# Kernel tuning notes

Hardware: AMD Instinct MI355X
Metric: run time of the kernel (lower is better)

The kernel has to match this reference:

```python
import jax, jax.numpy as jnp
import numpy as np

B, T, H, C = 1024, 1024, 128, 6  # batch, time, hidden_dim, output_dim


def setup_inputs() -> dict:
    key = jax.random.key(0)
    ks = jax.random.split(key, 16)
    xv = jax.random.normal(ks[0], (B, T, C), dtype=jnp.float32)
    m = (jax.random.uniform(ks[1], (B, T, C)) < 0.6).astype(jnp.float32)  # binary observed mask
    dt = jax.random.uniform(ks[2], (B, T, 1), dtype=jnp.float32) * 2.0    # positive time gaps
    x = jnp.concatenate([xv, m, dt], axis=-1)  # [B,T,13]
    s = 0.05
    return {
        "x": x,
        "x_mean": jnp.zeros((C,), jnp.float32),
        "decay_x_w": jnp.ones((C,), jnp.float32),
        "decay_x_b": jnp.zeros((C,), jnp.float32),
        "decay_h_w": jnp.ones((H,), jnp.float32),
        "decay_h_b": jnp.zeros((H,), jnp.float32),
        "w_ih": jax.random.normal(ks[3], (3 * H, 2 * C), jnp.float32) * s,
        "w_hh": jax.random.normal(ks[4], (3 * H, H), jnp.float32) * s,
        "b_ih": jnp.zeros((3 * H,), jnp.float32),
        "b_hh": jnp.zeros((3 * H,), jnp.float32),
        "w1": jax.random.normal(ks[5], (H, H), jnp.float32) * s,
        "b1": jnp.zeros((H,), jnp.float32),
        "w2": jax.random.normal(ks[6], (C, H), jnp.float32) * s,
        "b2": jnp.zeros((C,), jnp.float32),
        "wu1": jax.random.normal(ks[7], (H // 2, H), jnp.float32) * s,
        "bu1": jnp.zeros((H // 2,), jnp.float32),
        "wu2": jax.random.normal(ks[8], (C, H // 2), jnp.float32) * s,
        "bu2": jnp.zeros((C,), jnp.float32),
    }


def _grud_forward(x, x_mean, decay_x_w, decay_x_b, decay_h_w, decay_h_b,
                  w_ih, w_hh, b_ih, b_hh, w1, b1, w2, b2, wu1, bu1, wu2, bu2):
    xv = jnp.transpose(x[:, :, :C], (1, 0, 2))        # [T,B,C]
    m = jnp.transpose(x[:, :, C:2 * C], (1, 0, 2))    # [T,B,C]
    dt = jnp.transpose(x[:, :, 2 * C:2 * C + 1], (1, 0, 2))  # [T,B,1]

    def step(carry, inp):
        running, x_last, h = carry
        xv_t, m_t, dt_t = inp
        obs = m_t > 0.5
        running = jnp.where(obs, 0.0, running + dt_t)          # delta_t
        gamma_x = jnp.exp(-jax.nn.relu(running * decay_x_w + decay_x_b))  # [B,C]
        gamma_h = jnp.exp(-jax.nn.relu(dt_t * decay_h_w + decay_h_b))     # [B,H]
        h = gamma_h * h
        x_last = jnp.where(obs, xv_t, x_last)
        x_hat = m_t * xv_t + (1.0 - m_t) * (gamma_x * x_last + (1.0 - gamma_x) * x_mean)
        gru_in = jnp.concatenate([x_hat, m_t], axis=-1)        # [B,2C]
        gi = gru_in @ w_ih.T + b_ih                            # [B,3H]
        gh = h @ w_hh.T + b_hh                                 # [B,3H]
        i_r, i_z, i_n = jnp.split(gi, 3, axis=-1)
        h_r, h_z, h_n = jnp.split(gh, 3, axis=-1)
        r = jax.nn.sigmoid(i_r + h_r)
        z = jax.nn.sigmoid(i_z + h_z)
        n = jnp.tanh(i_n + r * h_n)
        h = (1.0 - z) * n + z * h
        pred = jax.nn.relu(h @ w1.T + b1) @ w2.T + b2
        unc = jax.nn.softplus(jax.nn.relu(h @ wu1.T + bu1) @ wu2.T + bu2)
        return (running, x_last, h), (pred, unc)

    bsz = x.shape[0]
    init = (jnp.zeros((bsz, C), x.dtype), jnp.zeros((bsz, C), x.dtype), jnp.zeros((bsz, H), x.dtype))
    _, (pred, unc) = jax.lax.scan(step, init, (xv, m, dt))
    return jnp.transpose(pred, (1, 0, 2)), jnp.transpose(unc, (1, 0, 2))


def reference(x, x_mean, decay_x_w, decay_x_b, decay_h_w, decay_h_b,
              w_ih, w_hh, b_ih, b_hh, w1, b1, w2, b2, wu1, bu1, wu2, bu2):
    return _grud_forward(x, x_mean, decay_x_w, decay_x_b, decay_h_w, decay_h_b,
                         w_ih, w_hh, b_ih, b_hh, w1, b1, w2, b2, wu1, bu1, wu2, bu2)
```

## Files before the change

### kernel.cpp

```cpp
#include <hip/hip_runtime.h>

namespace {
constexpr int NB = 1024, NT = 1024, NH = 128;
constexpr float L2E = 1.4426950408889634f;

typedef __bf16 bf16x8 __attribute__((ext_vector_type(8)));
typedef float  f32x4  __attribute__((ext_vector_type(4)));
typedef int    i32x4  __attribute__((ext_vector_type(4)));
union FRAG { i32x4 i; bf16x8 b; };

__device__ __forceinline__ unsigned short bfb(float f) {
  union { __bf16 h; unsigned short u; } c; c.h = (__bf16)f; return c.u;
}
__device__ __forceinline__ unsigned pkbf(float a, float b) {
  return (unsigned)bfb(a) | ((unsigned)bfb(b) << 16);
}
__device__ __forceinline__ unsigned long long pk4(const f32x4 v) {
  return (unsigned long long)pkbf(v[0], v[1]) |
         ((unsigned long long)pkbf(v[2], v[3]) << 32);
}
__device__ __forceinline__ float ex2(float x) { return __builtin_amdgcn_exp2f(x); }
__device__ __forceinline__ float rcp_(float x) { return __builtin_amdgcn_rcpf(x); }

__device__ __forceinline__ FRAG pk8(const float* pp, float sc) {
  FRAG f;
  #pragma unroll
  for (int j = 0; j < 4; ++j)
    f.i[j] = (int)pkbf(pp[2 * j] * sc, pp[2 * j + 1] * sc);
  return f;
}
}

#define MFMA(a, b, c) __builtin_amdgcn_mfma_f32_16x16x32_bf16(a, b, c, 0, 0, 0)
#define BAR() do { \
  asm volatile("s_waitcnt lgkmcnt(0)" ::: "memory"); \
  __builtin_amdgcn_s_barrier(); \
} while (0)

__global__ __launch_bounds__(512, 2)
void grud_combo(const float* __restrict__ x, const float* __restrict__ x_mean,
                const float* __restrict__ dxw, const float* __restrict__ dxb,
                const float* __restrict__ dhw, const float* __restrict__ dhb,
                const float* __restrict__ w_ih, const float* __restrict__ w_hh,
                const float* __restrict__ b_ih, const float* __restrict__ b_hh,
                const float* __restrict__ w1, const float* __restrict__ b1,
                const float* __restrict__ w2, const float* __restrict__ b2,
                const float* __restrict__ wu1, const float* __restrict__ bu1,
                const float* __restrict__ wu2, const float* __restrict__ bu2,
                float* __restrict__ out,
                char* __restrict__ hcur, const char* __restrict__ hprev,
                float* __restrict__ hstate, float* __restrict__ runst,
                float* __restrict__ xlst, int t0, int t0p, int Tc, int niter)
{
  __shared__ __align__(16) char lds[40960];

  const int tid = threadIdx.x;

  if (blockIdx.x < 64) {
    if (t0 >= NT) return;

    float (*xw)[16][17] = (float(*)[16][17])lds;
    unsigned short (*gin)[16][40] = (unsigned short(*)[16][40])(lds + 2176);
    char* hdL = lds + 4736;

    const int lane = tid & 63, wv = tid >> 6;
    const int lr = lane & 15, lg = lane >> 4;
    const int b0 = blockIdx.x * 16;
    const int uidx = wv * 16 + lr;
    const int uu0  = wv * 16 + 4 * lg;

    FRAG bhh[3][4], bgi[3];
    #pragma unroll
    for (int g = 0; g < 3; ++g) {
      const float sc = (g < 2) ? -L2E : 2.f * L2E;
      const int grow = g * 128 + uidx;
      const float* wrow = w_hh + (size_t)grow * NH;
      #pragma unroll
      for (int s = 0; s < 4; ++s) bhh[g][s] = pk8(wrow + 32 * s + 8 * lg, sc);
      FRAG f; f.i = i32x4{0, 0, 0, 0};
      if (lg < 2) {
        unsigned e[8];
        #pragma unroll
        for (int j = 0; j < 8; ++j) {
          const int c = 8 * lg + j; float v = 0.f;
          if (c < 12) {
            const int ch = c >> 1;
            v = ((c & 1) ? w_ih[(size_t)grow * 12 + 6 + ch]
                         : w_ih[(size_t)grow * 12 + ch]) * sc;
          } else if (c == 12) {
            v = ((g < 2) ? (b_ih[grow] + b_hh[grow]) : b_ih[grow]) * sc;
          }
          e[j] = bfb(v);
        }
        f.i[0] = (int)(e[0] | (e[1] << 16)); f.i[1] = (int)(e[2] | (e[3] << 16));
        f.i[2] = (int)(e[4] | (e[5] << 16)); f.i[3] = (int)(e[6] | (e[7] << 16));
      }
      bgi[g] = f;
    }
    f32x4 dhwV, dhbV, bhnV;
    #pragma unroll
    for (int r = 0; r < 4; ++r) {
      dhwV[r] = -L2E * dhw[uu0 + r];
      dhbV[r] = -L2E * dhb[uu0 + r];
      bhnV[r] = b_hh[256 + uu0 + r] * (2.f * L2E);
    }

    const int  item = wv * 24 + lane;
    const bool xl = (wv < 4) && (lane < 24);
    const int  xrow = item / 6, xch = item - 6 * (item / 6);
    float dxwS = 0.f, dxbS = 0.f, xm_l = 0.f, run = 0.f, xlast = 0.f;
    if (xl) {
      dxwS = -L2E * dxw[xch]; dxbS = -L2E * dxb[xch]; xm_l = x_mean[xch];
      if (t0 > 0) { run = runst[(b0 + xrow) * 6 + xch]; xlast = xlst[(b0 + xrow) * 6 + xch]; }
    }

    const bool sl = (tid >= 256) && (tid < 464);
    const int sid = tid - 256;
    const int rrow = sid / 13, rcc = sid - 13 * (sid / 13);
    const float* xbase = x + (size_t)(b0 + rrow) * (NT * 13) + rcc;

    f32x4 hn = {0.f, 0.f, 0.f, 0.f};
    if (t0 > 0) hn = *(const f32x4*)&hstate[(size_t)(b0 + lr) * NH + uu0];

    const int wOff = lr * 256 + (((2 * wv + (lg >> 1)) ^ (lr & 7)) << 4) + (lg & 1) * 8;
    int rOff[4];
    #pragma unroll
    for (int s = 0; s < 4; ++s) rOff[s] = lr * 256 + (((4 * s + lg) ^ (lr & 7)) << 4);

    for (int i = tid; i < 2 * 16 * 28; i += 512) {
      const int buf = i / 448, rem = i - 448 * buf;
      const int row = rem / 28, c = 12 + rem - 28 * (rem / 28);
      gin[buf][row][c] = (c == 12) ? (unsigned short)0x3F80 : (unsigned short)0;
    }

    const int cb0 = t0 & 1;
    if (sl) {
      xw[cb0][rrow][rcc]     = xbase[(size_t)t0 * 13];
      const int t1 = (t0 + 1 < NT) ? t0 + 1 : NT - 1;
      xw[cb0 ^ 1][rrow][rcc] = xbase[(size_t)t1 * 13];
    }
    __syncthreads();

    f32x4 hd;
    {
      const float dt0 = xw[cb0][lr][12];
      #pragma unroll
      for (int r = 0; r < 4; ++r)
        hd[r] = ex2(fminf(dt0 * dhwV[r] + dhbV[r], 0.f)) * hn[r];
      *(unsigned long long*)(hdL + cb0 * 4096 + wOff) = pk4(hd);
    }
    if (xl) {
      const float xv = xw[cb0][xrow][xch], mt = xw[cb0][xrow][6 + xch];
      const float dtv = xw[cb0][xrow][12];
      const bool obs = mt > 0.5f;
      run = obs ? 0.f : run + dtv;
      const float gx = ex2(fminf(run * dxwS + dxbS, 0.f));
      xlast = obs ? xv : xlast;
      const float xh = mt * xv + (1.f - mt) * (gx * xlast + (1.f - gx) * xm_l);
      ((unsigned*)&gin[cb0][xrow][0])[xch] = pkbf(xh, mt);
    }
    float xr2 = 0.f;
    if (sl) { const int t2 = (t0 + 2 < NT) ? t0 + 2 : NT - 1; xr2 = xbase[(size_t)t2 * 13]; }
    BAR();

    char* hwp = hcur + (((size_t)blockIdx.x * Tc) << 12) + wv * 32 + lg * 8 + lr * 256;
    const f32x4 z4 = {0.f, 0.f, 0.f, 0.f};
    const int tend = t0 + Tc;

    #pragma unroll 1
    for (int t = t0; t < tend; ++t) {
      const int p = t & 1, q = p ^ 1;

      FRAG ag; ag.i = *(const i32x4*)&gin[p][lr][8 * lg];
      FRAG ah[4];
      #pragma unroll
      for (int s = 0; s < 4; ++s)
        ah[s].i = *(const i32x4*)(hdL + p * 4096 + rOff[s]);
      const float dtn = xw[q][lr][12];

      if (sl) {
        xw[p][rrow][rcc] = xr2;
        xr2 = xbase[(size_t)((t + 3 < NT) ? t + 3 : NT - 1) * 13];
      }

      f32x4 accr = MFMA(bgi[0].b, ag.b, z4);
      f32x4 accz = MFMA(bgi[1].b, ag.b, z4);
      f32x4 ani  = MFMA(bgi[2].b, ag.b, z4);
      f32x4 anh  = z4;
      #pragma unroll
      for (int s = 0; s < 4; ++s) {
        accr = MFMA(bhh[0][s].b, ah[s].b, accr);
        accz = MFMA(bhh[1][s].b, ah[s].b, accz);
        anh  = MFMA(bhh[2][s].b, ah[s].b, anh);
      }

      f32x4 hbv = anh + bhnV;
      #pragma unroll
      for (int r = 0; r < 4; ++r) {
        const float Er = ex2(accr[r]);
        const float rr = rcp_(1.f + Er);
        const float na = __builtin_fmaf(rr, hbv[r], ani[r]);
        const float En = ex2(na);
        const float Ez = ex2(accz[r]);
        const float em1 = En - 1.f, ep1 = En + 1.f;
        const float num = __builtin_fmaf(hd[r], ep1, em1 * Ez);
        const float den = ep1 * (1.f + Ez);
        hn[r] = num * rcp_(den);
      }

      *(unsigned long long*)hwp = pk4(hn);
      hwp += 4096;

      #pragma unroll
      for (int r = 0; r < 4; ++r)
        hd[r] = ex2(fminf(dtn * dhwV[r] + dhbV[r], 0.f)) * hn[r];
      *(unsigned long long*)(hdL + q * 4096 + wOff) = pk4(hd);

      if (xl && t + 1 < tend) {
        const float xv = xw[q][xrow][xch], mt = xw[q][xrow][6 + xch];
        const float dtv = xw[q][xrow][12];
        const bool obs = mt > 0.5f;
        run = obs ? 0.f : run + dtv;
        const float gx = ex2(fminf(run * dxwS + dxbS, 0.f));
        xlast = obs ? xv : xlast;
        const float xh = mt * xv + (1.f - mt) * (gx * xlast + (1.f - gx) * xm_l);
        ((unsigned*)&gin[q][xrow][0])[xch] = pkbf(xh, mt);
      }
      BAR();
    }

    *(f32x4*)&hstate[(size_t)(b0 + lr) * NH + uu0] = hn;
    if (xl) { runst[(b0 + xrow) * 6 + xch] = run; xlst[(b0 + xrow) * 6 + xch] = xlast; }

  } else {
    if (t0p < 0) return;

    const int hb = blockIdx.x - 64;
    const int tid2 = tid & 255, half = tid >> 8;
    const int lane2 = tid2 & 63, w4 = tid2 >> 6;
    const int lr = lane2 & 15, lg = lane2 >> 4;
    char* ldsH = lds + half * 20480;

    FRAG bw1a[4], bw1b[4], bq1[4], bw2[4], bq2[2];
    #pragma unroll
    for (int s = 0; s < 4; ++s) {
      bw1a[s] = pk8(w1 + (size_t)((2 * w4) * 16 + lr) * 128 + 32 * s + 8 * lg, 1.f);
      bw1b[s] = pk8(w1 + (size_t)((2 * w4 + 1) * 16 + lr) * 128 + 32 * s + 8 * lg, 1.f);
      bq1[s]  = pk8(wu1 + (size_t)(w4 * 16 + lr) * 128 + 32 * s + 8 * lg, 1.f);
      if (lr < 6) bw2[s] = pk8(w2 + (size_t)lr * 128 + 32 * s + 8 * lg, 1.f);
      else        bw2[s].i = i32x4{0, 0, 0, 0};
      if (s < 2) {
        if (lr < 6) bq2[s] = pk8(wu2 + (size_t)lr * 64 + 32 * s + 8 * lg, 1.f);
        else        bq2[s].i = i32x4{0, 0, 0, 0};
      }
    }
    const float b1a = b1[(2 * w4) * 16 + lr], b1b = b1[(2 * w4 + 1) * 16 + lr];
    const float bu1l = bu1[w4 * 16 + lr];
    const float b2l = (lr < 6) ? b2[lr] : 0.f, bu2l = (lr < 6) ? bu2[lr] : 0.f;
    const f32x4 z4 = {0.f, 0.f, 0.f, 0.f};

    const int tc2 = Tc >> 1, total = 64 * tc2;
    const int cy0 = (2 * w4) * 16 + lr, cy1 = (2 * w4 + 1) * 16 + lr;
    const int cu = w4 * 16 + lr;

    #pragma unroll 1
    for (int it = 0; it < niter; ++it) {
      const int hu = it * 384 + hb * 2 + half;
      const bool valid = hu < total;
      int chain = 0, tp = 0;
      if (valid) { chain = hu / tc2; tp = hu - chain * tc2; }

      if (valid) {
        const char* src = hprev + (((size_t)chain * Tc + tp * 2) << 12);
        const int o = tid2 * 16, row = o >> 8, cell = (o >> 4) & 15;
        #pragma unroll
        for (int k2 = 0; k2 < 2; ++k2) {
          uint4 v = *(const uint4*)(src + k2 * 4096 + o);
          *(uint4*)(ldsH + k2 * 4096 + row * 256 + ((cell ^ (row & 7)) << 4)) = v;
        }
      }
      __syncthreads();

      if (valid) {
        #pragma unroll
        for (int k = 0; k < 2; ++k) {
          FRAG A[4];
          #pragma unroll
          for (int s = 0; s < 4; ++s)
            A[s].i = *(const i32x4*)(ldsH + k * 4096 + lr * 256 +
                                     (((4 * s + lg) ^ (lr & 7)) << 4));
          f32x4 aa = z4, ab = z4, au = z4;
          #pragma unroll
          for (int s = 0; s < 4; ++s) {
            aa = MFMA(A[s].b, bw1a[s].b, aa);
            ab = MFMA(A[s].b, bw1b[s].b, ab);
            au = MFMA(A[s].b, bq1[s].b, au);
          }
          #pragma unroll
          for (int r = 0; r < 4; ++r) {
            const int m = k * 16 + 4 * lg + r;
            *(unsigned short*)(ldsH + 8192 + m * 256 + (((cy0 >> 3) ^ (m & 7)) << 4) +
                               (cy0 & 7) * 2) = bfb(fmaxf(aa[r] + b1a, 0.f));
            *(unsigned short*)(ldsH + 8192 + m * 256 + (((cy1 >> 3) ^ (m & 7)) << 4) +
                               (cy1 & 7) * 2) = bfb(fmaxf(ab[r] + b1b, 0.f));
            *(unsigned short*)(ldsH + 16384 + m * 128 + (((cu >> 3) ^ (m & 7)) << 4) +
                               (cu & 7) * 2) = bfb(fmaxf(au[r] + bu1l, 0.f));
          }
        }
      }
      __syncthreads();

      if (valid && w4 < 2) {
        const int mrow = w4 * 16 + lr;
        FRAG Y[4], U[2];
        #pragma unroll
        for (int s = 0; s < 4; ++s)
          Y[s].i = *(const i32x4*)(ldsH + 8192 + mrow * 256 +
                                   (((4 * s + lg) ^ (lr & 7)) << 4));
        #pragma unroll
        for (int s = 0; s < 2; ++s)
          U[s].i = *(const i32x4*)(ldsH + 16384 + mrow * 128 +
                                   (((4 * s + lg) ^ (lr & 7)) << 4));
        f32x4 ap = z4, aq = z4;
        #pragma unroll
        for (int s = 0; s < 4; ++s) ap = MFMA(Y[s].b, bw2[s].b, ap);
        #pragma unroll
        for (int s = 0; s < 2; ++s) aq = MFMA(U[s].b, bq2[s].b, aq);

        if (lr < 6) {
          const int t = t0p + tp * 2 + w4;
          #pragma unroll
          for (int r = 0; r < 4; ++r) {
            const int b = chain * 16 + 4 * lg + r;
            const size_t o = ((size_t)b * NT + t) * 6 + lr;
            out[o] = ap[r] + b2l;
            const float xa = aq[r] + bu2l;
            const float sp = fmaxf(xa, 0.f) + 0.6931471805599453f *
                __builtin_amdgcn_logf(1.f + ex2(-fabsf(xa) * L2E));
            out[(size_t)NB * NT * 6 + o] = sp;
          }
        }
      }
      __syncthreads();
    }
  }
}

extern "C" void kernel_launch(void* const* d_in, const int* in_sizes, int n_in,
                              void* d_out, int out_size, void* d_ws, size_t ws_size,
                              hipStream_t stream) {
  (void)in_sizes; (void)n_in; (void)out_size;
  const float* p[18];
  for (int i = 0; i < 18; ++i) p[i] = (const float*)d_in[i];

  const size_t STATE = (size_t)1024 * 128 * 4 + 2 * (size_t)1024 * 6 * 4;
  int Tc = 256;
  while (Tc > 16 && (2 * ((size_t)Tc << 18) + STATE) > ws_size) Tc >>= 1;

  char* h0 = (char*)d_ws;
  char* h1 = h0 + ((size_t)Tc << 18);
  float* hstate = (float*)(h1 + ((size_t)Tc << 18));
  float* runst = hstate + 1024 * 128;
  float* xlst = runst + 1024 * 6;

  const int nch = NT / Tc;
  const int niter = (64 * (Tc / 2) + 383) / 384;

  for (int k = 0; k <= nch; ++k) {
    char* hcur = (k & 1) ? h1 : h0;
    const char* hprev = (k & 1) ? h0 : h1;
    hipLaunchKernelGGL(grud_combo, dim3(256), dim3(512), 0, stream,
                       p[0], p[1], p[2], p[3], p[4], p[5], p[6], p[7], p[8], p[9],
                       p[10], p[11], p[12], p[13], p[14], p[15], p[16], p[17],
                       (float*)d_out, hcur, hprev, hstate, runst, xlst,
                       k * Tc, (k - 1) * Tc, Tc, niter);
  }
}
```

Measured before the change: 879.4 us.

## Concentrate GRU recurrence on four waves and offload input prep to helper waves

```diff
diff --git a/kernel.cpp b/kernel.cpp
--- a/kernel.cpp
+++ b/kernel.cpp
@@ -55,6 +55,8 @@
   __shared__ __align__(16) char lds[40960];
 
   const int tid = threadIdx.x;
+  const int lane = tid & 63, wv = tid >> 6;
+  const int lr = lane & 15, lg = lane >> 4;
 
   if (blockIdx.x < 64) {
     if (t0 >= NT) return;
@@ -63,67 +65,85 @@
     unsigned short (*gin)[16][40] = (unsigned short(*)[16][40])(lds + 2176);
     char* hdL = lds + 4736;
 
-    const int lane = tid & 63, wv = tid >> 6;
-    const int lr = lane & 15, lg = lane >> 4;
     const int b0 = blockIdx.x * 16;
-    const int uidx = wv * 16 + lr;
-    const int uu0  = wv * 16 + 4 * lg;
-
-    FRAG bhh[3][4], bgi[3];
-    #pragma unroll
-    for (int g = 0; g < 3; ++g) {
-      const float sc = (g < 2) ? -L2E : 2.f * L2E;
-      const int grow = g * 128 + uidx;
-      const float* wrow = w_hh + (size_t)grow * NH;
+    const bool gw = (wv < 4);
+    const int uB = (wv & 3) * 32;
+
+    FRAG whh[3][2][4], wgi[3][2];
+    f32x4 dhwV[2], dhbV[2], bhnV[2];
+    if (gw) {
       #pragma unroll
-      for (int s = 0; s < 4; ++s) bhh[g][s] = pk8(wrow + 32 * s + 8 * lg, sc);
-      FRAG f; f.i = i32x4{0, 0, 0, 0};
-      if (lg < 2) {
-        unsigned e[8];
-        #pragma unroll
-        for (int j = 0; j < 8; ++j) {
-          const int c = 8 * lg + j; float v = 0.f;
-          if (c < 12) {
-            const int ch = c >> 1;
-            v = ((c & 1) ? w_ih[(size_t)grow * 12 + 6 + ch]
-                         : w_ih[(size_t)grow * 12 + ch]) * sc;
-          } else if (c == 12) {
-            v = ((g < 2) ? (b_ih[grow] + b_hh[grow]) : b_ih[grow]) * sc;
-          }
-          e[j] = bfb(v);
-        }
-        f.i[0] = (int)(e[0] | (e[1] << 16)); f.i[1] = (int)(e[2] | (e[3] << 16));
-        f.i[2] = (int)(e[4] | (e[5] << 16)); f.i[3] = (int)(e[6] | (e[7] << 16));
-      }
-      bgi[g] = f;
-    }
-    f32x4 dhwV, dhbV, bhnV;
-    #pragma unroll
-    for (int r = 0; r < 4; ++r) {
-      dhwV[r] = -L2E * dhw[uu0 + r];
-      dhbV[r] = -L2E * dhb[uu0 + r];
-      bhnV[r] = b_hh[256 + uu0 + r] * (2.f * L2E);
-    }
-
-    const int  item = wv * 24 + lane;
-    const bool xl = (wv < 4) && (lane < 24);
-    const int  xrow = item / 6, xch = item - 6 * (item / 6);
+      for (int g = 0; g < 3; ++g) {
+        const float sc = (g < 2) ? -L2E : 2.f * L2E;
+        #pragma unroll
+        for (int tau = 0; tau < 2; ++tau) {
+          const int grow = g * 128 + uB + 16 * tau + lr;
+          const float* wrow = w_hh + (size_t)grow * NH;
+          #pragma unroll
+          for (int s = 0; s < 4; ++s)
+            whh[g][tau][s] = pk8(wrow + 32 * s + 8 * lg, sc);
+          FRAG f; f.i = i32x4{0, 0, 0, 0};
+          if (lg < 2) {
+            unsigned e[8];
+            #pragma unroll
+            for (int j = 0; j < 8; ++j) {
+              const int c = 8 * lg + j; float v = 0.f;
+              if (c < 12) {
+                const int ch = c >> 1;
+                v = ((c & 1) ? w_ih[(size_t)grow * 12 + 6 + ch]
+                             : w_ih[(size_t)grow * 12 + ch]) * sc;
+              } else if (c == 12) {
+                v = ((g < 2) ? (b_ih[grow] + b_hh[grow]) : b_ih[grow]) * sc;
+              }
+              e[j] = bfb(v);
+            }
+            f.i[0] = (int)(e[0] | (e[1] << 16)); f.i[1] = (int)(e[2] | (e[3] << 16));
+            f.i[2] = (int)(e[4] | (e[5] << 16)); f.i[3] = (int)(e[6] | (e[7] << 16));
+          }
+          wgi[g][tau] = f;
+        }
+      }
+      #pragma unroll
+      for (int tau = 0; tau < 2; ++tau) {
+        const int u0 = uB + 16 * tau + 4 * lg;
+        #pragma unroll
+        for (int r = 0; r < 4; ++r) {
+          dhwV[tau][r] = -L2E * dhw[u0 + r];
+          dhbV[tau][r] = -L2E * dhb[u0 + r];
+          bhnV[tau][r] = b_hh[256 + u0 + r] * (2.f * L2E);
+        }
+      }
+    }
+
+    const int xi = (wv - 4) * 64 + lane;
+    const bool xl = (wv == 4) || (wv == 5 && lane < 32);
+    const int xrow = xi / 6, xch = xi - 6 * (xi / 6);
     float dxwS = 0.f, dxbS = 0.f, xm_l = 0.f, run = 0.f, xlast = 0.f;
     if (xl) {
       dxwS = -L2E * dxw[xch]; dxbS = -L2E * dxb[xch]; xm_l = x_mean[xch];
       if (t0 > 0) { run = runst[(b0 + xrow) * 6 + xch]; xlast = xlst[(b0 + xrow) * 6 + xch]; }
     }
 
-    const bool sl = (tid >= 256) && (tid < 464);
-    const int sid = tid - 256;
-    const int rrow = sid / 13, rcc = sid - 13 * (sid / 13);
-    const float* xbase = x + (size_t)(b0 + rrow) * (NT * 13) + rcc;
-
-    f32x4 hn = {0.f, 0.f, 0.f, 0.f};
-    if (t0 > 0) hn = *(const f32x4*)&hstate[(size_t)(b0 + lr) * NH + uu0];
-
-    const int wOff = lr * 256 + (((2 * wv + (lg >> 1)) ^ (lr & 7)) << 4) + (lg & 1) * 8;
-    int rOff[4];
+    const int sid = (wv - 6) * 64 + lane;
+    const bool s1 = (wv >= 6);
+    const bool s2 = s1 && (sid < 80);
+    const int r1r = sid / 13, r1c = sid - 13 * r1r;
+    const int r2r = (sid + 128) / 13, r2c = (sid + 128) - 13 * r2r;
+    const float* xb1 = x + (size_t)(b0 + r1r) * (NT * 13) + r1c;
+    const float* xb2 = x + (size_t)(b0 + r2r) * (NT * 13) + r2c;
+
+    f32x4 hn0 = {0.f,0.f,0.f,0.f}, hn1 = {0.f,0.f,0.f,0.f};
+    if (gw && t0 > 0) {
+      hn0 = *(const f32x4*)&hstate[(size_t)(b0 + lr) * NH + uB + 4 * lg];
+      hn1 = *(const f32x4*)&hstate[(size_t)(b0 + lr) * NH + uB + 16 + 4 * lg];
+    }
+
+    int wOffT[2], rOff[4];
+    #pragma unroll
+    for (int tau = 0; tau < 2; ++tau) {
+      const int cell = ((uB + 16 * tau + 4 * lg) >> 3);
+      wOffT[tau] = lr * 256 + ((cell ^ (lr & 7)) << 4) + (lg & 1) * 8;
+    }
     #pragma unroll
     for (int s = 0; s < 4; ++s) rOff[s] = lr * 256 + (((4 * s + lg) ^ (lr & 7)) << 4);
 
@@ -134,20 +154,27 @@
     }
 
     const int cb0 = t0 & 1;
-    if (sl) {
-      xw[cb0][rrow][rcc]     = xbase[(size_t)t0 * 13];
+    if (s1) {
       const int t1 = (t0 + 1 < NT) ? t0 + 1 : NT - 1;
-      xw[cb0 ^ 1][rrow][rcc] = xbase[(size_t)t1 * 13];
+      xw[cb0][r1r][r1c]     = xb1[(size_t)t0 * 13];
+      xw[cb0 ^ 1][r1r][r1c] = xb1[(size_t)t1 * 13];
+      if (s2) {
+        xw[cb0][r2r][r2c]     = xb2[(size_t)t0 * 13];
+        xw[cb0 ^ 1][r2r][r2c] = xb2[(size_t)t1 * 13];
+      }
     }
     __syncthreads();
 
-    f32x4 hd;
-    {
+    f32x4 hd0, hd1;
+    if (gw) {
       const float dt0 = xw[cb0][lr][12];
       #pragma unroll
-      for (int r = 0; r < 4; ++r)
-        hd[r] = ex2(fminf(dt0 * dhwV[r] + dhbV[r], 0.f)) * hn[r];
-      *(unsigned long long*)(hdL + cb0 * 4096 + wOff) = pk4(hd);
+      for (int r = 0; r < 4; ++r) {
+        hd0[r] = ex2(fminf(dt0 * dhwV[0][r] + dhbV[0][r], 0.f)) * hn0[r];
+        hd1[r] = ex2(fminf(dt0 * dhwV[1][r] + dhbV[1][r], 0.f)) * hn1[r];
+      }
+      *(unsigned long long*)(hdL + cb0 * 4096 + wOffT[0]) = pk4(hd0);
+      *(unsigned long long*)(hdL + cb0 * 4096 + wOffT[1]) = pk4(hd1);
     }
     if (xl) {
       const float xv = xw[cb0][xrow][xch], mt = xw[cb0][xrow][6 + xch];
@@ -159,11 +186,15 @@
       const float xh = mt * xv + (1.f - mt) * (gx * xlast + (1.f - gx) * xm_l);
       ((unsigned*)&gin[cb0][xrow][0])[xch] = pkbf(xh, mt);
     }
-    float xr2 = 0.f;
-    if (sl) { const int t2 = (t0 + 2 < NT) ? t0 + 2 : NT - 1; xr2 = xbase[(size_t)t2 * 13]; }
+    float xr2a = 0.f, xr2b = 0.f;
+    if (s1) {
+      const int t2 = (t0 + 2 < NT) ? t0 + 2 : NT - 1;
+      xr2a = xb1[(size_t)t2 * 13];
+      if (s2) xr2b = xb2[(size_t)t2 * 13];
+    }
     BAR();
 
-    char* hwp = hcur + (((size_t)blockIdx.x * Tc) << 12) + wv * 32 + lg * 8 + lr * 256;
+    char* hwp = hcur + (((size_t)blockIdx.x * Tc) << 12) + lr * 256 + (uB + 4 * lg) * 2;
     const f32x4 z4 = {0.f, 0.f, 0.f, 0.f};
     const int tend = t0 + Tc;
 
@@ -171,65 +202,97 @@
     for (int t = t0; t < tend; ++t) {
       const int p = t & 1, q = p ^ 1;
 
-      FRAG ag; ag.i = *(const i32x4*)&gin[p][lr][8 * lg];
-      FRAG ah[4];
-      #pragma unroll
-      for (int s = 0; s < 4; ++s)
-        ah[s].i = *(const i32x4*)(hdL + p * 4096 + rOff[s]);
-      const float dtn = xw[q][lr][12];
-
-      if (sl) {
-        xw[p][rrow][rcc] = xr2;
-        xr2 = xbase[(size_t)((t + 3 < NT) ? t + 3 : NT - 1) * 13];
-      }
-
-      f32x4 accr = MFMA(bgi[0].b, ag.b, z4);
-      f32x4 accz = MFMA(bgi[1].b, ag.b, z4);
-      f32x4 ani  = MFMA(bgi[2].b, ag.b, z4);
-      f32x4 anh  = z4;
-      #pragma unroll
-      for (int s = 0; s < 4; ++s) {
-        accr = MFMA(bhh[0][s].b, ah[s].b, accr);
-        accz = MFMA(bhh[1][s].b, ah[s].b, accz);
-        anh  = MFMA(bhh[2][s].b, ah[s].b, anh);
-      }
-
-      f32x4 hbv = anh + bhnV;
-      #pragma unroll
-      for (int r = 0; r < 4; ++r) {
-        const float Er = ex2(accr[r]);
-        const float rr = rcp_(1.f + Er);
-        const float na = __builtin_fmaf(rr, hbv[r], ani[r]);
-        const float En = ex2(na);
-        const float Ez = ex2(accz[r]);
-        const float em1 = En - 1.f, ep1 = En + 1.f;
-        const float num = __builtin_fmaf(hd[r], ep1, em1 * Ez);
-        const float den = ep1 * (1.f + Ez);
-        hn[r] = num * rcp_(den);
-      }
-
-      *(unsigned long long*)hwp = pk4(hn);
+      if (gw) {
+        const float dtn = xw[q][lr][12];
+        f32x4 gm0, gm1;
+        #pragma unroll
+        for (int r = 0; r < 4; ++r) {
+          gm0[r] = ex2(fminf(dtn * dhwV[0][r] + dhbV[0][r], 0.f));
+          gm1[r] = ex2(fminf(dtn * dhwV[1][r] + dhbV[1][r], 0.f));
+        }
+
+        FRAG ag; ag.i = *(const i32x4*)&gin[p][lr][8 * lg];
+        FRAG ah[4];
+        #pragma unroll
+        for (int s = 0; s < 4; ++s)
+          ah[s].i = *(const i32x4*)(hdL + p * 4096 + rOff[s]);
+
+        f32x4 r0 = MFMA(wgi[0][0].b, ag.b, z4);
+        f32x4 zz0 = MFMA(wgi[1][0].b, ag.b, z4);
+        f32x4 ni0 = MFMA(wgi[2][0].b, ag.b, z4);
+        f32x4 nh0 = z4;
+        f32x4 r1 = MFMA(wgi[0][1].b, ag.b, z4);
+        f32x4 zz1 = MFMA(wgi[1][1].b, ag.b, z4);
+        f32x4 ni1 = MFMA(wgi[2][1].b, ag.b, z4);
+        f32x4 nh1 = z4;
+        #pragma unroll
+        for (int s = 0; s < 4; ++s) {
+          r0  = MFMA(whh[0][0][s].b, ah[s].b, r0);
+          zz0 = MFMA(whh[1][0][s].b, ah[s].b, zz0);
+          nh0 = MFMA(whh[2][0][s].b, ah[s].b, nh0);
+          r1  = MFMA(whh[0][1][s].b, ah[s].b, r1);
+          zz1 = MFMA(whh[1][1][s].b, ah[s].b, zz1);
+          nh1 = MFMA(whh[2][1][s].b, ah[s].b, nh1);
+        }
+
+        f32x4 hb0 = nh0 + bhnV[0], hb1 = nh1 + bhnV[1];
+        #pragma unroll
+        for (int r = 0; r < 4; ++r) {
+          {
+            const float Er = ex2(r0[r]);
+            const float rr = rcp_(1.f + Er);
+            const float na = __builtin_fmaf(rr, hb0[r], ni0[r]);
+            const float En = ex2(na);
+            const float Ez = ex2(zz0[r]);
+            const float em1 = En - 1.f, ep1 = En + 1.f;
+            const float num = __builtin_fmaf(hd0[r], ep1, em1 * Ez);
+            hn0[r] = num * rcp_(ep1 * (1.f + Ez));
+          }
+          {
+            const float Er = ex2(r1[r]);
+            const float rr = rcp_(1.f + Er);
+            const float na = __builtin_fmaf(rr, hb1[r], ni1[r]);
+            const float En = ex2(na);
+            const float Ez = ex2(zz1[r]);
+            const float em1 = En - 1.f, ep1 = En + 1.f;
+            const float num = __builtin_fmaf(hd1[r], ep1, em1 * Ez);
+            hn1[r] = num * rcp_(ep1 * (1.f + Ez));
+          }
+        }
+
+        *(unsigned long long*)hwp = pk4(hn0);
+        *(unsigned long long*)(hwp + 32) = pk4(hn1);
+
+        #pragma unroll
+        for (int r = 0; r < 4; ++r) { hd0[r] = gm0[r] * hn0[r]; hd1[r] = gm1[r] * hn1[r]; }
+        *(unsigned long long*)(hdL + q * 4096 + wOffT[0]) = pk4(hd0);
+        *(unsigned long long*)(hdL + q * 4096 + wOffT[1]) = pk4(hd1);
+      } else {
+        if (xl && t + 1 < tend) {
+          const float xv = xw[q][xrow][xch], mt = xw[q][xrow][6 + xch];
+          const float dtv = xw[q][xrow][12];
+          const bool obs = mt > 0.5f;
+          run = obs ? 0.f : run + dtv;
+          const float gx = ex2(fminf(run * dxwS + dxbS, 0.f));
+          xlast = obs ? xv : xlast;
+          const float xh = mt * xv + (1.f - mt) * (gx * xlast + (1.f - gx) * xm_l);
+          ((unsigned*)&gin[q][xrow][0])[xch] = pkbf(xh, mt);
+        }
+        if (s1) {
+          const int t3 = (t + 3 < NT) ? t + 3 : NT - 1;
+          xw[p][r1r][r1c] = xr2a;
+          xr2a = xb1[(size_t)t3 * 13];
+          if (s2) { xw[p][r2r][r2c] = xr2b; xr2b = xb2[(size_t)t3 * 13]; }
+        }
+      }
       hwp += 4096;
-
-      #pragma unroll
-      for (int r = 0; r < 4; ++r)
-        hd[r] = ex2(fminf(dtn * dhwV[r] + dhbV[r], 0.f)) * hn[r];
-      *(unsigned long long*)(hdL + q * 4096 + wOff) = pk4(hd);
-
-      if (xl && t + 1 < tend) {
-        const float xv = xw[q][xrow][xch], mt = xw[q][xrow][6 + xch];
-        const float dtv = xw[q][xrow][12];
-        const bool obs = mt > 0.5f;
-        run = obs ? 0.f : run + dtv;
-        const float gx = ex2(fminf(run * dxwS + dxbS, 0.f));
-        xlast = obs ? xv : xlast;
-        const float xh = mt * xv + (1.f - mt) * (gx * xlast + (1.f - gx) * xm_l);
-        ((unsigned*)&gin[q][xrow][0])[xch] = pkbf(xh, mt);
-      }
       BAR();
     }
 
-    *(f32x4*)&hstate[(size_t)(b0 + lr) * NH + uu0] = hn;
+    if (gw) {
+      *(f32x4*)&hstate[(size_t)(b0 + lr) * NH + uB + 4 * lg] = hn0;
+      *(f32x4*)&hstate[(size_t)(b0 + lr) * NH + uB + 16 + 4 * lg] = hn1;
+    }
     if (xl) { runst[(b0 + xrow) * 6 + xch] = run; xlst[(b0 + xrow) * 6 + xch] = xlast; }
 
   } else {
@@ -238,30 +301,30 @@
     const int hb = blockIdx.x - 64;
     const int tid2 = tid & 255, half = tid >> 8;
     const int lane2 = tid2 & 63, w4 = tid2 >> 6;
-    const int lr = lane2 & 15, lg = lane2 >> 4;
+    const int lr2 = lane2 & 15, lg2 = lane2 >> 4;
     char* ldsH = lds + half * 20480;
 
     FRAG bw1a[4], bw1b[4], bq1[4], bw2[4], bq2[2];
     #pragma unroll
     for (int s = 0; s < 4; ++s) {
-      bw1a[s] = pk8(w1 + (size_t)((2 * w4) * 16 + lr) * 128 + 32 * s + 8 * lg, 1.f);
-      bw1b[s] = pk8(w1 + (size_t)((2 * w4 + 1) * 16 + lr) * 128 + 32 * s + 8 * lg, 1.f);
-      bq1[s]  = pk8(wu1 + (size_t)(w4 * 16 + lr) * 128 + 32 * s + 8 * lg, 1.f);
-      if (lr < 6) bw2[s] = pk8(w2 + (size_t)lr * 128 + 32 * s + 8 * lg, 1.f);
-      else        bw2[s].i = i32x4{0, 0, 0, 0};
+      bw1a[s] = pk8(w1 + (size_t)((2 * w4) * 16 + lr2) * 128 + 32 * s + 8 * lg2, 1.f);
+      bw1b[s] = pk8(w1 + (size_t)((2 * w4 + 1) * 16 + lr2) * 128 + 32 * s + 8 * lg2, 1.f);
+      bq1[s]  = pk8(wu1 + (size_t)(w4 * 16 + lr2) * 128 + 32 * s + 8 * lg2, 1.f);
+      if (lr2 < 6) bw2[s] = pk8(w2 + (size_t)lr2 * 128 + 32 * s + 8 * lg2, 1.f);
+      else         bw2[s].i = i32x4{0, 0, 0, 0};
       if (s < 2) {
-        if (lr < 6) bq2[s] = pk8(wu2 + (size_t)lr * 64 + 32 * s + 8 * lg, 1.f);
-        else        bq2[s].i = i32x4{0, 0, 0, 0};
-      }
-    }
-    const float b1a = b1[(2 * w4) * 16 + lr], b1b = b1[(2 * w4 + 1) * 16 + lr];
-    const float bu1l = bu1[w4 * 16 + lr];
-    const float b2l = (lr < 6) ? b2[lr] : 0.f, bu2l = (lr < 6) ? bu2[lr] : 0.f;
+        if (lr2 < 6) bq2[s] = pk8(wu2 + (size_t)lr2 * 64 + 32 * s + 8 * lg2, 1.f);
+        else         bq2[s].i = i32x4{0, 0, 0, 0};
+      }
+    }
+    const float b1a = b1[(2 * w4) * 16 + lr2], b1b = b1[(2 * w4 + 1) * 16 + lr2];
+    const float bu1l = bu1[w4 * 16 + lr2];
+    const float b2l = (lr2 < 6) ? b2[lr2] : 0.f, bu2l = (lr2 < 6) ? bu2[lr2] : 0.f;
     const f32x4 z4 = {0.f, 0.f, 0.f, 0.f};
 
     const int tc2 = Tc >> 1, total = 64 * tc2;
-    const int cy0 = (2 * w4) * 16 + lr, cy1 = (2 * w4 + 1) * 16 + lr;
-    const int cu = w4 * 16 + lr;
+    const int cy0 = (2 * w4) * 16 + lr2, cy1 = (2 * w4 + 1) * 16 + lr2;
+    const int cu = w4 * 16 + lr2;
 
     #pragma unroll 1
     for (int it = 0; it < niter; ++it) {
@@ -287,8 +350,8 @@
           FRAG A[4];
           #pragma unroll
           for (int s = 0; s < 4; ++s)
-            A[s].i = *(const i32x4*)(ldsH + k * 4096 + lr * 256 +
-                                     (((4 * s + lg) ^ (lr & 7)) << 4));
+            A[s].i = *(const i32x4*)(ldsH + k * 4096 + lr2 * 256 +
+                                     (((4 * s + lg2) ^ (lr2 & 7)) << 4));
           f32x4 aa = z4, ab = z4, au = z4;
           #pragma unroll
           for (int s = 0; s < 4; ++s) {
@@ -298,7 +361,7 @@
           }
           #pragma unroll
           for (int r = 0; r < 4; ++r) {
-            const int m = k * 16 + 4 * lg + r;
+            const int m = k * 16 + 4 * lg2 + r;
             *(unsigned short*)(ldsH + 8192 + m * 256 + (((cy0 >> 3) ^ (m & 7)) << 4) +
                                (cy0 & 7) * 2) = bfb(fmaxf(aa[r] + b1a, 0.f));
             *(unsigned short*)(ldsH + 8192 + m * 256 + (((cy1 >> 3) ^ (m & 7)) << 4) +
@@ -311,28 +374,28 @@
       __syncthreads();
 
       if (valid && w4 < 2) {
-        const int mrow = w4 * 16 + lr;
+        const int mrow = w4 * 16 + lr2;
         FRAG Y[4], U[2];
         #pragma unroll
         for (int s = 0; s < 4; ++s)
           Y[s].i = *(const i32x4*)(ldsH + 8192 + mrow * 256 +
-                                   (((4 * s + lg) ^ (lr & 7)) << 4));
+                                   (((4 * s + lg2) ^ (lr2 & 7)) << 4));
         #pragma unroll
         for (int s = 0; s < 2; ++s)
           U[s].i = *(const i32x4*)(ldsH + 16384 + mrow * 128 +
-                                   (((4 * s + lg) ^ (lr & 7)) << 4));
+                                   (((4 * s + lg2) ^ (lr2 & 7)) << 4));
         f32x4 ap = z4, aq = z4;
         #pragma unroll
         for (int s = 0; s < 4; ++s) ap = MFMA(Y[s].b, bw2[s].b, ap);
         #pragma unroll
         for (int s = 0; s < 2; ++s) aq = MFMA(U[s].b, bq2[s].b, aq);
 
-        if (lr < 6) {
+        if (lr2 < 6) {
           const int t = t0p + tp * 2 + w4;
           #pragma unroll
           for (int r = 0; r < 4; ++r) {
-            const int b = chain * 16 + 4 * lg + r;
-            const size_t o = ((size_t)b * NT + t) * 6 + lr;
+            const int b = chain * 16 + 4 * lg2 + r;
+            const size_t o = ((size_t)b * NT + t) * 6 + lr2;
             out[o] = ap[r] + b2l;
             const float xa = aq[r] + bu2l;
             const float sp = fmaxf(xa, 0.f) + 0.6931471805599453f *
```

Result: slower. 927.7 us (+5.5%).

## Process two 16-row batch chains per recurrence block, freeing blocks for the head

Applied to the files above, without the earlier changes.

```diff
diff --git a/kernel.cpp b/kernel.cpp
--- a/kernel.cpp
+++ b/kernel.cpp
@@ -55,17 +55,17 @@
   __shared__ __align__(16) char lds[40960];
 
   const int tid = threadIdx.x;
-
-  if (blockIdx.x < 64) {
+  const int lane = tid & 63, wv = tid >> 6;
+  const int lr = lane & 15, lg = lane >> 4;
+
+  if (blockIdx.x < 32) {
     if (t0 >= NT) return;
 
-    float (*xw)[16][17] = (float(*)[16][17])lds;
-    unsigned short (*gin)[16][40] = (unsigned short(*)[16][40])(lds + 2176);
-    char* hdL = lds + 4736;
-
-    const int lane = tid & 63, wv = tid >> 6;
-    const int lr = lane & 15, lg = lane >> 4;
-    const int b0 = blockIdx.x * 16;
+    float (*xw)[32][17] = (float(*)[32][17])lds;
+    unsigned short (*gin)[32][40] = (unsigned short(*)[32][40])(lds + 4352);
+    char* hdL = lds + 9472;
+
+    const int b0 = blockIdx.x * 32;
     const int uidx = wv * 16 + lr;
     const int uu0  = wv * 16 + 4 * lg;
 
@@ -105,49 +105,58 @@
       bhnV[r] = b_hh[256 + uu0 + r] * (2.f * L2E);
     }
 
-    const int  item = wv * 24 + lane;
-    const bool xl = (wv < 4) && (lane < 24);
-    const int  xrow = item / 6, xch = item - 6 * (item / 6);
+    const bool xl = (wv < 3);
+    const int xi = wv * 64 + lane;
+    const int xrow = xi / 6, xch = xi - 6 * (xi / 6);
     float dxwS = 0.f, dxbS = 0.f, xm_l = 0.f, run = 0.f, xlast = 0.f;
     if (xl) {
       dxwS = -L2E * dxw[xch]; dxbS = -L2E * dxb[xch]; xm_l = x_mean[xch];
       if (t0 > 0) { run = runst[(b0 + xrow) * 6 + xch]; xlast = xlst[(b0 + xrow) * 6 + xch]; }
     }
 
-    const bool sl = (tid >= 256) && (tid < 464);
     const int sid = tid - 256;
-    const int rrow = sid / 13, rcc = sid - 13 * (sid / 13);
-    const float* xbase = x + (size_t)(b0 + rrow) * (NT * 13) + rcc;
-
-    f32x4 hn = {0.f, 0.f, 0.f, 0.f};
-    if (t0 > 0) hn = *(const f32x4*)&hstate[(size_t)(b0 + lr) * NH + uu0];
+    const bool sl = (sid >= 0) && (sid < 208);
+    const int rr_ = sid / 13, rc_ = sid - 13 * rr_;
+    const float* xbA = x + (size_t)(b0 + rr_) * (NT * 13) + rc_;
+    const float* xbB = x + (size_t)(b0 + 16 + rr_) * (NT * 13) + rc_;
+
+    f32x4 hnA = {0.f,0.f,0.f,0.f}, hnB = {0.f,0.f,0.f,0.f};
+    if (t0 > 0) {
+      hnA = *(const f32x4*)&hstate[(size_t)(b0 + lr) * NH + uu0];
+      hnB = *(const f32x4*)&hstate[(size_t)(b0 + 16 + lr) * NH + uu0];
+    }
 
     const int wOff = lr * 256 + (((2 * wv + (lg >> 1)) ^ (lr & 7)) << 4) + (lg & 1) * 8;
     int rOff[4];
     #pragma unroll
     for (int s = 0; s < 4; ++s) rOff[s] = lr * 256 + (((4 * s + lg) ^ (lr & 7)) << 4);
 
-    for (int i = tid; i < 2 * 16 * 28; i += 512) {
-      const int buf = i / 448, rem = i - 448 * buf;
+    for (int i = tid; i < 2 * 32 * 28; i += 512) {
+      const int buf = i / 896, rem = i - 896 * buf;
       const int row = rem / 28, c = 12 + rem - 28 * (rem / 28);
       gin[buf][row][c] = (c == 12) ? (unsigned short)0x3F80 : (unsigned short)0;
     }
 
     const int cb0 = t0 & 1;
     if (sl) {
-      xw[cb0][rrow][rcc]     = xbase[(size_t)t0 * 13];
       const int t1 = (t0 + 1 < NT) ? t0 + 1 : NT - 1;
-      xw[cb0 ^ 1][rrow][rcc] = xbase[(size_t)t1 * 13];
+      xw[cb0][rr_][rc_]          = xbA[(size_t)t0 * 13];
+      xw[cb0 ^ 1][rr_][rc_]      = xbA[(size_t)t1 * 13];
+      xw[cb0][16 + rr_][rc_]     = xbB[(size_t)t0 * 13];
+      xw[cb0 ^ 1][16 + rr_][rc_] = xbB[(size_t)t1 * 13];
     }
     __syncthreads();
 
-    f32x4 hd;
+    f32x4 hdA, hdB;
     {
-      const float dt0 = xw[cb0][lr][12];
-      #pragma unroll
-      for (int r = 0; r < 4; ++r)
-        hd[r] = ex2(fminf(dt0 * dhwV[r] + dhbV[r], 0.f)) * hn[r];
-      *(unsigned long long*)(hdL + cb0 * 4096 + wOff) = pk4(hd);
+      const float dtA = xw[cb0][lr][12], dtB = xw[cb0][16 + lr][12];
+      #pragma unroll
+      for (int r = 0; r < 4; ++r) {
+        hdA[r] = ex2(fminf(dtA * dhwV[r] + dhbV[r], 0.f)) * hnA[r];
+        hdB[r] = ex2(fminf(dtB * dhwV[r] + dhbV[r], 0.f)) * hnB[r];
+      }
+      *(unsigned long long*)(hdL + cb0 * 8192 + wOff) = pk4(hdA);
+      *(unsigned long long*)(hdL + cb0 * 8192 + 4096 + wOff) = pk4(hdB);
     }
     if (xl) {
       const float xv = xw[cb0][xrow][xch], mt = xw[cb0][xrow][6 + xch];
@@ -159,11 +168,16 @@
       const float xh = mt * xv + (1.f - mt) * (gx * xlast + (1.f - gx) * xm_l);
       ((unsigned*)&gin[cb0][xrow][0])[xch] = pkbf(xh, mt);
     }
-    float xr2 = 0.f;
-    if (sl) { const int t2 = (t0 + 2 < NT) ? t0 + 2 : NT - 1; xr2 = xbase[(size_t)t2 * 13]; }
+    float xr2a = 0.f, xr2b = 0.f;
+    if (sl) {
+      const int t2 = (t0 + 2 < NT) ? t0 + 2 : NT - 1;
+      xr2a = xbA[(size_t)t2 * 13]; xr2b = xbB[(size_t)t2 * 13];
+    }
     BAR();
 
-    char* hwp = hcur + (((size_t)blockIdx.x * Tc) << 12) + wv * 32 + lg * 8 + lr * 256;
+    const int chainA = blockIdx.x * 2;
+    char* hwpA = hcur + (((size_t)chainA * Tc) << 12) + lr * 256 + wv * 32 + lg * 8;
+    char* hwpB = hwpA + ((size_t)Tc << 12);
     const f32x4 z4 = {0.f, 0.f, 0.f, 0.f};
     const int tend = t0 + Tc;
 
@@ -171,50 +185,61 @@
     for (int t = t0; t < tend; ++t) {
       const int p = t & 1, q = p ^ 1;
 
-      FRAG ag; ag.i = *(const i32x4*)&gin[p][lr][8 * lg];
-      FRAG ah[4];
-      #pragma unroll
-      for (int s = 0; s < 4; ++s)
-        ah[s].i = *(const i32x4*)(hdL + p * 4096 + rOff[s]);
-      const float dtn = xw[q][lr][12];
-
-      if (sl) {
-        xw[p][rrow][rcc] = xr2;
-        xr2 = xbase[(size_t)((t + 3 < NT) ? t + 3 : NT - 1) * 13];
-      }
-
-      f32x4 accr = MFMA(bgi[0].b, ag.b, z4);
-      f32x4 accz = MFMA(bgi[1].b, ag.b, z4);
-      f32x4 ani  = MFMA(bgi[2].b, ag.b, z4);
-      f32x4 anh  = z4;
+      const float dtnA = xw[q][lr][12], dtnB = xw[q][16 + lr][12];
+      f32x4 gmA, gmB;
+      #pragma unroll
+      for (int r = 0; r < 4; ++r) {
+        gmA[r] = ex2(fminf(dtnA * dhwV[r] + dhbV[r], 0.f));
+        gmB[r] = ex2(fminf(dtnB * dhwV[r] + dhbV[r], 0.f));
+      }
+
+      FRAG agA, agB, ahA[4], ahB[4];
+      agA.i = *(const i32x4*)&gin[p][lr][8 * lg];
+      agB.i = *(const i32x4*)&gin[p][16 + lr][8 * lg];
       #pragma unroll
       for (int s = 0; s < 4; ++s) {
-        accr = MFMA(bhh[0][s].b, ah[s].b, accr);
-        accz = MFMA(bhh[1][s].b, ah[s].b, accz);
-        anh  = MFMA(bhh[2][s].b, ah[s].b, anh);
-      }
-
-      f32x4 hbv = anh + bhnV;
+        ahA[s].i = *(const i32x4*)(hdL + p * 8192 + rOff[s]);
+        ahB[s].i = *(const i32x4*)(hdL + p * 8192 + 4096 + rOff[s]);
+      }
+
+      f32x4 rA = MFMA(bgi[0].b, agA.b, z4), rB = MFMA(bgi[0].b, agB.b, z4);
+      f32x4 zA = MFMA(bgi[1].b, agA.b, z4), zB = MFMA(bgi[1].b, agB.b, z4);
+      f32x4 niA = MFMA(bgi[2].b, agA.b, z4), niB = MFMA(bgi[2].b, agB.b, z4);
+      f32x4 nhA = z4, nhB = z4;
+      #pragma unroll
+      for (int s = 0; s < 4; ++s) {
+        rA  = MFMA(bhh[0][s].b, ahA[s].b, rA);
+        rB  = MFMA(bhh[0][s].b, ahB[s].b, rB);
+        zA  = MFMA(bhh[1][s].b, ahA[s].b, zA);
+        zB  = MFMA(bhh[1][s].b, ahB[s].b, zB);
+        nhA = MFMA(bhh[2][s].b, ahA[s].b, nhA);
+        nhB = MFMA(bhh[2][s].b, ahB[s].b, nhB);
+      }
+
+      f32x4 hbA = nhA + bhnV, hbB = nhB + bhnV;
       #pragma unroll
       for (int r = 0; r < 4; ++r) {
-        const float Er = ex2(accr[r]);
-        const float rr = rcp_(1.f + Er);
-        const float na = __builtin_fmaf(rr, hbv[r], ani[r]);
-        const float En = ex2(na);
-        const float Ez = ex2(accz[r]);
-        const float em1 = En - 1.f, ep1 = En + 1.f;
-        const float num = __builtin_fmaf(hd[r], ep1, em1 * Ez);
-        const float den = ep1 * (1.f + Ez);
-        hn[r] = num * rcp_(den);
-      }
-
-      *(unsigned long long*)hwp = pk4(hn);
-      hwp += 4096;
-
-      #pragma unroll
-      for (int r = 0; r < 4; ++r)
-        hd[r] = ex2(fminf(dtn * dhwV[r] + dhbV[r], 0.f)) * hn[r];
-      *(unsigned long long*)(hdL + q * 4096 + wOff) = pk4(hd);
+        const float ErA = ex2(rA[r]), ErB = ex2(rB[r]);
+        const float rrA = rcp_(1.f + ErA), rrB = rcp_(1.f + ErB);
+        const float naA = __builtin_fmaf(rrA, hbA[r], niA[r]);
+        const float naB = __builtin_fmaf(rrB, hbB[r], niB[r]);
+        const float EnA = ex2(naA), EnB = ex2(naB);
+        const float EzA = ex2(zA[r]), EzB = ex2(zB[r]);
+        const float ep1A = EnA + 1.f, ep1B = EnB + 1.f;
+        const float numA = __builtin_fmaf(hdA[r], ep1A, (EnA - 1.f) * EzA);
+        const float numB = __builtin_fmaf(hdB[r], ep1B, (EnB - 1.f) * EzB);
+        hnA[r] = numA * rcp_(ep1A * (1.f + EzA));
+        hnB[r] = numB * rcp_(ep1B * (1.f + EzB));
+      }
+
+      *(unsigned long long*)hwpA = pk4(hnA);
+      *(unsigned long long*)hwpB = pk4(hnB);
+      hwpA += 4096; hwpB += 4096;
+
+      #pragma unroll
+      for (int r = 0; r < 4; ++r) { hdA[r] = gmA[r] * hnA[r]; hdB[r] = gmB[r] * hnB[r]; }
+      *(unsigned long long*)(hdL + q * 8192 + wOff) = pk4(hdA);
+      *(unsigned long long*)(hdL + q * 8192 + 4096 + wOff) = pk4(hdB);
 
       if (xl && t + 1 < tend) {
         const float xv = xw[q][xrow][xch], mt = xw[q][xrow][6 + xch];
@@ -226,46 +251,52 @@
         const float xh = mt * xv + (1.f - mt) * (gx * xlast + (1.f - gx) * xm_l);
         ((unsigned*)&gin[q][xrow][0])[xch] = pkbf(xh, mt);
       }
+      if (sl) {
+        const int t3 = (t + 3 < NT) ? t + 3 : NT - 1;
+        xw[p][rr_][rc_] = xr2a;      xr2a = xbA[(size_t)t3 * 13];
+        xw[p][16 + rr_][rc_] = xr2b; xr2b = xbB[(size_t)t3 * 13];
+      }
       BAR();
     }
 
-    *(f32x4*)&hstate[(size_t)(b0 + lr) * NH + uu0] = hn;
+    *(f32x4*)&hstate[(size_t)(b0 + lr) * NH + uu0] = hnA;
+    *(f32x4*)&hstate[(size_t)(b0 + 16 + lr) * NH + uu0] = hnB;
     if (xl) { runst[(b0 + xrow) * 6 + xch] = run; xlst[(b0 + xrow) * 6 + xch] = xlast; }
 
   } else {
     if (t0p < 0) return;
 
-    const int hb = blockIdx.x - 64;
+    const int hb = blockIdx.x - 32;
     const int tid2 = tid & 255, half = tid >> 8;
     const int lane2 = tid2 & 63, w4 = tid2 >> 6;
-    const int lr = lane2 & 15, lg = lane2 >> 4;
+    const int lr2 = lane2 & 15, lg2 = lane2 >> 4;
     char* ldsH = lds + half * 20480;
 
     FRAG bw1a[4], bw1b[4], bq1[4], bw2[4], bq2[2];
     #pragma unroll
     for (int s = 0; s < 4; ++s) {
-      bw1a[s] = pk8(w1 + (size_t)((2 * w4) * 16 + lr) * 128 + 32 * s + 8 * lg, 1.f);
-      bw1b[s] = pk8(w1 + (size_t)((2 * w4 + 1) * 16 + lr) * 128 + 32 * s + 8 * lg, 1.f);
-      bq1[s]  = pk8(wu1 + (size_t)(w4 * 16 + lr) * 128 + 32 * s + 8 * lg, 1.f);
-      if (lr < 6) bw2[s] = pk8(w2 + (size_t)lr * 128 + 32 * s + 8 * lg, 1.f);
-      else        bw2[s].i = i32x4{0, 0, 0, 0};
+      bw1a[s] = pk8(w1 + (size_t)((2 * w4) * 16 + lr2) * 128 + 32 * s + 8 * lg2, 1.f);
+      bw1b[s] = pk8(w1 + (size_t)((2 * w4 + 1) * 16 + lr2) * 128 + 32 * s + 8 * lg2, 1.f);
+      bq1[s]  = pk8(wu1 + (size_t)(w4 * 16 + lr2) * 128 + 32 * s + 8 * lg2, 1.f);
+      if (lr2 < 6) bw2[s] = pk8(w2 + (size_t)lr2 * 128 + 32 * s + 8 * lg2, 1.f);
+      else         bw2[s].i = i32x4{0, 0, 0, 0};
       if (s < 2) {
-        if (lr < 6) bq2[s] = pk8(wu2 + (size_t)lr * 64 + 32 * s + 8 * lg, 1.f);
-        else        bq2[s].i = i32x4{0, 0, 0, 0};
-      }
-    }
-    const float b1a = b1[(2 * w4) * 16 + lr], b1b = b1[(2 * w4 + 1) * 16 + lr];
-    const float bu1l = bu1[w4 * 16 + lr];
-    const float b2l = (lr < 6) ? b2[lr] : 0.f, bu2l = (lr < 6) ? bu2[lr] : 0.f;
+        if (lr2 < 6) bq2[s] = pk8(wu2 + (size_t)lr2 * 64 + 32 * s + 8 * lg2, 1.f);
+        else         bq2[s].i = i32x4{0, 0, 0, 0};
+      }
+    }
+    const float b1a = b1[(2 * w4) * 16 + lr2], b1b = b1[(2 * w4 + 1) * 16 + lr2];
+    const float bu1l = bu1[w4 * 16 + lr2];
+    const float b2l = (lr2 < 6) ? b2[lr2] : 0.f, bu2l = (lr2 < 6) ? bu2[lr2] : 0.f;
     const f32x4 z4 = {0.f, 0.f, 0.f, 0.f};
 
     const int tc2 = Tc >> 1, total = 64 * tc2;
-    const int cy0 = (2 * w4) * 16 + lr, cy1 = (2 * w4 + 1) * 16 + lr;
-    const int cu = w4 * 16 + lr;
+    const int cy0 = (2 * w4) * 16 + lr2, cy1 = (2 * w4 + 1) * 16 + lr2;
+    const int cu = w4 * 16 + lr2;
 
     #pragma unroll 1
     for (int it = 0; it < niter; ++it) {
-      const int hu = it * 384 + hb * 2 + half;
+      const int hu = it * 448 + hb * 2 + half;
       const bool valid = hu < total;
       int chain = 0, tp = 0;
       if (valid) { chain = hu / tc2; tp = hu - chain * tc2; }
@@ -287,8 +318,8 @@
           FRAG A[4];
           #pragma unroll
           for (int s = 0; s < 4; ++s)
-            A[s].i = *(const i32x4*)(ldsH + k * 4096 + lr * 256 +
-                                     (((4 * s + lg) ^ (lr & 7)) << 4));
+            A[s].i = *(const i32x4*)(ldsH + k * 4096 + lr2 * 256 +
+                                     (((4 * s + lg2) ^ (lr2 & 7)) << 4));
           f32x4 aa = z4, ab = z4, au = z4;
           #pragma unroll
           for (int s = 0; s < 4; ++s) {
@@ -298,7 +329,7 @@
           }
           #pragma unroll
           for (int r = 0; r < 4; ++r) {
-            const int m = k * 16 + 4 * lg + r;
+            const int m = k * 16 + 4 * lg2 + r;
             *(unsigned short*)(ldsH + 8192 + m * 256 + (((cy0 >> 3) ^ (m & 7)) << 4) +
                                (cy0 & 7) * 2) = bfb(fmaxf(aa[r] + b1a, 0.f));
             *(unsigned short*)(ldsH + 8192 + m * 256 + (((cy1 >> 3) ^ (m & 7)) << 4) +
@@ -311,28 +342,28 @@
       __syncthreads();
 
       if (valid && w4 < 2) {
-        const int mrow = w4 * 16 + lr;
+        const int mrow = w4 * 16 + lr2;
         FRAG Y[4], U[2];
         #pragma unroll
         for (int s = 0; s < 4; ++s)
           Y[s].i = *(const i32x4*)(ldsH + 8192 + mrow * 256 +
-                                   (((4 * s + lg) ^ (lr & 7)) << 4));
+                                   (((4 * s + lg2) ^ (lr2 & 7)) << 4));
         #pragma unroll
         for (int s = 0; s < 2; ++s)
           U[s].i = *(const i32x4*)(ldsH + 16384 + mrow * 128 +
-                                   (((4 * s + lg) ^ (lr & 7)) << 4));
+                                   (((4 * s + lg2) ^ (lr2 & 7)) << 4));
         f32x4 ap = z4, aq = z4;
         #pragma unroll
         for (int s = 0; s < 4; ++s) ap = MFMA(Y[s].b, bw2[s].b, ap);
         #pragma unroll
         for (int s = 0; s < 2; ++s) aq = MFMA(U[s].b, bq2[s].b, aq);
 
-        if (lr < 6) {
+        if (lr2 < 6) {
           const int t = t0p + tp * 2 + w4;
           #pragma unroll
           for (int r = 0; r < 4; ++r) {
-            const int b = chain * 16 + 4 * lg + r;
-            const size_t o = ((size_t)b * NT + t) * 6 + lr;
+            const int b = chain * 16 + 4 * lg2 + r;
+            const size_t o = ((size_t)b * NT + t) * 6 + lr2;
             out[o] = ap[r] + b2l;
             const float xa = aq[r] + bu2l;
             const float sp = fmaxf(xa, 0.f) + 0.6931471805599453f *
@@ -364,7 +395,7 @@
   float* xlst = runst + 1024 * 6;
 
   const int nch = NT / Tc;
-  const int niter = (64 * (Tc / 2) + 383) / 384;
+  const int niter = (64 * (Tc / 2) + 447) / 448;
 
   for (int k = 0; k <= nch; ++k) {
     char* hcur = (k & 1) ? h1 : h0;
```

Measured after the change: 1.481 ms. +68.4%, slower.
